# Kernel optimization log

Hardware: AMD Instinct MI355X
Metric: run time of the kernel (lower is better)

## Reference

```python
import jax, jax.numpy as jnp
import numpy as np

MIDC = 256
HEADS = 16
HEADC = MIDC // HEADS
EPS = 1e-5


def _layernorm(x, w, b):
    # Faithful to the custom torch LayerNorm: unbiased std (ddof=1) and
    # division by (std + eps), NOT sqrt(var + eps).
    mean = jnp.mean(x, axis=-1, keepdims=True)
    std = jnp.std(x, axis=-1, keepdims=True, ddof=1)
    return w * (x - mean) / (std + EPS) + b


def setup_inputs() -> dict:
    key = jax.random.key(0)
    ks = jax.random.split(key, 3)
    B, HW = 8, 16384
    x = jax.random.normal(ks[0], (B, HW, MIDC), dtype=jnp.float32)
    W_qkv = jax.random.normal(ks[1], (3 * MIDC, MIDC), dtype=jnp.float32) * 0.02
    b_qkv = jnp.zeros((3 * MIDC,), dtype=jnp.float32)
    kln_w = jnp.ones((HEADS, 1, HEADC), dtype=jnp.float32)
    kln_b = jnp.zeros((HEADS, 1, HEADC), dtype=jnp.float32)
    vln_w = jnp.ones((HEADS, 1, HEADC), dtype=jnp.float32)
    vln_b = jnp.zeros((HEADS, 1, HEADC), dtype=jnp.float32)
    W_proj = jax.random.normal(ks[2], (MIDC, MIDC), dtype=jnp.float32) * 0.02
    b_proj = jnp.zeros((MIDC,), dtype=jnp.float32)
    return {"x": x, "W_qkv": W_qkv, "b_qkv": b_qkv,
            "kln_w": kln_w, "kln_b": kln_b, "vln_w": vln_w, "vln_b": vln_b,
            "W_proj": W_proj, "b_proj": b_proj}


def reference(x, W_qkv, b_qkv, kln_w, kln_b, vln_w, vln_b, W_proj, b_proj):
    B, HW, C = x.shape
    bias = x
    # QKV projection -> [B, heads, HW, 3*headc]
    qkv = (jnp.einsum('bnc,oc->bno', x, W_qkv) + b_qkv)
    qkv = qkv.reshape(B, HW, HEADS, 3 * HEADC).transpose(0, 2, 1, 3)
    q, k, v = jnp.split(qkv, 3, axis=-1)  # each [B, heads, HW, headc]
    k = _layernorm(k, kln_w, kln_b)
    v = _layernorm(v, vln_w, vln_b)
    # linear attention: kv = k^T v / HW, then q @ kv
    kv = jnp.einsum('bhnd,bhne->bhde', k, v) / HW  # [B, heads, headc, headc]
    out = jnp.einsum('bhnd,bhde->bhne', q, kv)     # [B, heads, HW, headc]
    out = out.transpose(0, 2, 1, 3).reshape(B, HW, C)
    ret = out + bias
    proj = jnp.einsum('bnc,oc->bno', ret, W_proj) + b_proj
    return jax.nn.gelu(proj, approximate=False) + bias
```

## Files before the change

### kernel.cpp

```cpp
#include <hip/hip_runtime.h>
#include <hip/hip_bf16.h>
#include <math.h>


#define EPSF 1e-5f

typedef __bf16 bf16x8 __attribute__((ext_vector_type(8)));
typedef __bf16 bf16x4 __attribute__((ext_vector_type(4)));
typedef float  f32x4  __attribute__((ext_vector_type(4)));

__global__ void k0_prep(const float* __restrict__ Wqkv, const float* __restrict__ Wproj,
                        __bf16* __restrict__ Wkv, __bf16* __restrict__ Wp,
                        float* __restrict__ kv) {
  int idx = blockIdx.x * 256 + threadIdx.x;
  if (idx < 32768) kv[idx] = 0.f;
  {
    int r = idx >> 8, c = idx & 255;
    int half = r >> 8;
    int rr = r & 255;
    int h = rr >> 4, d = rr & 15;
    Wkv[idx] = (__bf16)Wqkv[(h*48 + 16 + half*16 + d)*256 + c];
  }
  if (idx < 65536) Wp[idx] = (__bf16)Wproj[idx];
}

__launch_bounds__(512, 4)
__global__ void k1a(const float* __restrict__ x, const __bf16* __restrict__ Wkv,
                    const float* __restrict__ bqkv,
                    const float* __restrict__ klnw, const float* __restrict__ klnb,
                    const float* __restrict__ vlnw, const float* __restrict__ vlnb,
                    float* __restrict__ kvout) {
  __shared__ __align__(16) char smem[70656];
  __bf16 (*xs)[264] = reinterpret_cast<__bf16(*)[264]>(smem);
  const int tid = threadIdx.x;
  const int w = tid >> 6, l = tid & 63, lr = l & 15, g = l >> 4;
  __bf16 (*tTk)[72] = reinterpret_cast<__bf16(*)[72]>(smem + 33792 + w*4608);
  __bf16 (*tTv)[64] = reinterpret_cast<__bf16(*)[64]>(smem + w*4096);

  const long row0 = (long)blockIdx.x * 64;
  const int b = (int)(row0 >> 14);

  #pragma unroll
  for (int i = 0; i < 8; ++i) {
    int idx = tid + i*512;
    int r = idx >> 6, c4 = (idx & 63) << 2;
    f32x4 v = *reinterpret_cast<const f32x4*>(x + (row0 + r)*256 + c4);
    bf16x4 pk; pk[0]=(__bf16)v[0]; pk[1]=(__bf16)v[1]; pk[2]=(__bf16)v[2]; pk[3]=(__bf16)v[3];
    *reinterpret_cast<bf16x4*>(&xs[r][c4]) = pk;
  }

  bf16x8 wk[2][8];
  #pragma unroll
  for (int cb=0;cb<2;cb++) {
    const __bf16* wp = Wkv + (size_t)(w*32 + cb*16 + lr)*256 + g*8;
    #pragma unroll
    for (int kc=0;kc<8;kc++) wk[cb][kc] = *reinterpret_cast<const bf16x8*>(wp + kc*32);
  }
  __syncthreads();

  f32x4 acc[2][4];
  for (int cb=0;cb<2;cb++) for (int rb=0;rb<4;rb++)
    for (int j=0;j<4;j++) acc[cb][rb][j]=0.f;
  #pragma unroll
  for (int kc = 0; kc < 8; ++kc) {
    const int kb = kc*32 + g*8;
    bf16x8 bf_[4];
    #pragma unroll
    for (int rb=0;rb<4;rb++)
      bf_[rb] = *reinterpret_cast<const bf16x8*>(&xs[rb*16+lr][kb]);
    #pragma unroll
    for (int cb=0;cb<2;cb++)
      #pragma unroll
      for (int rb=0;rb<4;rb++)
        acc[cb][rb] = __builtin_amdgcn_mfma_f32_16x16x32_bf16(wk[cb][kc], bf_[rb], acc[cb][rb], 0,0,0);
  }

  bf16x8 wv[2][8];
  #pragma unroll
  for (int cb=0;cb<2;cb++) {
    const __bf16* wp = Wkv + (size_t)(256 + w*32 + cb*16 + lr)*256 + g*8;
    #pragma unroll
    for (int kc=0;kc<8;kc++) wv[cb][kc] = *reinterpret_cast<const bf16x8*>(wp + kc*32);
  }

  #pragma unroll
  for (int cb=0;cb<2;cb++) {
    const int h = 2*w + cb;
    const f32x4 bb  = *reinterpret_cast<const f32x4*>(bqkv + h*48 + 16 + 4*g);
    const f32x4 lwv = *reinterpret_cast<const f32x4*>(klnw + h*16 + 4*g);
    const f32x4 lbv = *reinterpret_cast<const f32x4*>(klnb + h*16 + 4*g);
    #pragma unroll
    for (int rb=0;rb<4;rb++) {
      float v0 = acc[cb][rb][0] + bb[0];
      float v1 = acc[cb][rb][1] + bb[1];
      float v2 = acc[cb][rb][2] + bb[2];
      float v3 = acc[cb][rb][3] + bb[3];
      float sum = v0+v1+v2+v3;
      sum += __shfl_xor(sum, 16); sum += __shfl_xor(sum, 32);
      const float mu = sum * 0.0625f;
      const float d0=v0-mu, d1=v1-mu, d2=v2-mu, d3=v3-mu;
      float q = d0*d0 + d1*d1 + d2*d2 + d3*d3;
      q += __shfl_xor(q, 16); q += __shfl_xor(q, 32);
      const float sc = __frsqrt_rn(q * (1.f/15.f));
      const int rr = rb*16 + lr;
      tTk[cb*16 + 4*g+0][rr] = (__bf16)(lwv[0]*d0*sc + lbv[0]);
      tTk[cb*16 + 4*g+1][rr] = (__bf16)(lwv[1]*d1*sc + lbv[1]);
      tTk[cb*16 + 4*g+2][rr] = (__bf16)(lwv[2]*d2*sc + lbv[2]);
      tTk[cb*16 + 4*g+3][rr] = (__bf16)(lwv[3]*d3*sc + lbv[3]);
    }
  }

  for (int cb=0;cb<2;cb++) for (int rb=0;rb<4;rb++)
    for (int j=0;j<4;j++) acc[cb][rb][j]=0.f;
  #pragma unroll
  for (int kc = 0; kc < 8; ++kc) {
    const int kb = kc*32 + g*8;
    bf16x8 bf_[4];
    #pragma unroll
    for (int rb=0;rb<4;rb++)
      bf_[rb] = *reinterpret_cast<const bf16x8*>(&xs[rb*16+lr][kb]);
    #pragma unroll
    for (int cb=0;cb<2;cb++)
      #pragma unroll
      for (int rb=0;rb<4;rb++)
        acc[cb][rb] = __builtin_amdgcn_mfma_f32_16x16x32_bf16(wv[cb][kc], bf_[rb], acc[cb][rb], 0,0,0);
  }

  bf16x4 vpk[2][4];
  #pragma unroll
  for (int cb=0;cb<2;cb++) {
    const int h = 2*w + cb;
    const f32x4 bb  = *reinterpret_cast<const f32x4*>(bqkv + h*48 + 32 + 4*g);
    const f32x4 lwv = *reinterpret_cast<const f32x4*>(vlnw + h*16 + 4*g);
    const f32x4 lbv = *reinterpret_cast<const f32x4*>(vlnb + h*16 + 4*g);
    #pragma unroll
    for (int rb=0;rb<4;rb++) {
      float v0 = acc[cb][rb][0] + bb[0];
      float v1 = acc[cb][rb][1] + bb[1];
      float v2 = acc[cb][rb][2] + bb[2];
      float v3 = acc[cb][rb][3] + bb[3];
      float sum = v0+v1+v2+v3;
      sum += __shfl_xor(sum, 16); sum += __shfl_xor(sum, 32);
      const float mu = sum * 0.0625f;
      const float d0=v0-mu, d1=v1-mu, d2=v2-mu, d3=v3-mu;
      float q = d0*d0 + d1*d1 + d2*d2 + d3*d3;
      q += __shfl_xor(q, 16); q += __shfl_xor(q, 32);
      const float sc = __frsqrt_rn(q * (1.f/15.f));
      vpk[cb][rb][0] = (__bf16)(lwv[0]*d0*sc + lbv[0]);
      vpk[cb][rb][1] = (__bf16)(lwv[1]*d1*sc + lbv[1]);
      vpk[cb][rb][2] = (__bf16)(lwv[2]*d2*sc + lbv[2]);
      vpk[cb][rb][3] = (__bf16)(lwv[3]*d3*sc + lbv[3]);
    }
  }

  __syncthreads();

  #pragma unroll
  for (int cb=0;cb<2;cb++) {
    #pragma unroll
    for (int rb=0;rb<4;rb++) {
      const int rr = rb*16 + lr;
      tTv[cb*16 + 4*g+0][rr ^ (((4*g+0)&7)<<3)] = vpk[cb][rb][0];
      tTv[cb*16 + 4*g+1][rr ^ (((4*g+1)&7)<<3)] = vpk[cb][rb][1];
      tTv[cb*16 + 4*g+2][rr ^ (((4*g+2)&7)<<3)] = vpk[cb][rb][2];
      tTv[cb*16 + 4*g+3][rr ^ (((4*g+3)&7)<<3)] = vpk[cb][rb][3];
    }
  }

  #pragma unroll
  for (int hh=0; hh<2; ++hh) {
    f32x4 c; c[0]=0.f; c[1]=0.f; c[2]=0.f; c[3]=0.f;
    #pragma unroll
    for (int ch=0; ch<2; ++ch) {
      const int s = ch*32 + g*8;
      bf16x8 a  = *reinterpret_cast<const bf16x8*>(&tTk[hh*16 + lr][s]);
      bf16x8 bv = *reinterpret_cast<const bf16x8*>(&tTv[hh*16 + lr][s ^ ((lr&7)<<3)]);
      c = __builtin_amdgcn_mfma_f32_16x16x32_bf16(a, bv, c, 0,0,0);
    }
    float* dst = kvout + ((size_t)(b*16 + 2*w + hh) << 8);
    #pragma unroll
    for (int j=0;j<4;j++)
      atomicAdd(dst + (4*g+j)*16 + lr, c[j]);
  }
}

__global__ void k2_weff(const float* __restrict__ Wqkv, const float* __restrict__ bqkv,
                        const float* __restrict__ kvin,
                        __bf16* __restrict__ Wqe, float* __restrict__ beff) {
  const int b = blockIdx.x >> 4, h = blockIdx.x & 15;
  const int c = threadIdx.x;
  __shared__ float kvs[16][16];
  kvs[c >> 4][c & 15] = kvin[(b*16 + h)*256 + c] * (1.f/16384.f);
  __syncthreads();
  #pragma unroll 4
  for (int e=0;e<16;e++) {
    float acc = 0.f;
    #pragma unroll
    for (int d=0; d<16; d++)
      acc += kvs[d][e] * Wqkv[(h*48 + d)*256 + c];
    Wqe[((size_t)b*256 + h*16 + e)*256 + c] = (__bf16)acc;
  }
  if (c < 16) {
    float acc = 0.f;
    #pragma unroll
    for (int d=0; d<16; d++) acc += kvs[d][c] * bqkv[h*48 + d];
    beff[b*256 + h*16 + c] = acc;
  }
}

__launch_bounds__(512, 4)
__global__ void k3_fused(const float* __restrict__ x, const __bf16* __restrict__ Wqe,
                         const float* __restrict__ beff, const __bf16* __restrict__ Wp,
                         const float* __restrict__ bproj, float* __restrict__ out) {
  __shared__ __align__(16) __bf16 xs[64][264];
  __shared__ __align__(16) char rsraw[33792];
  __bf16 (*rs)[264] = reinterpret_cast<__bf16(*)[264]>(rsraw);
  float  (*fst)[260] = reinterpret_cast<float(*)[260]>(rsraw);
  const int tid = threadIdx.x;
  const long browg = (long)blockIdx.x * 64;
  const int b = (int)(browg >> 14);
  const int w = tid>>6, l = tid&63, lr = l&15, g = l>>4;

  #pragma unroll
  for (int i = 0; i < 8; ++i) {
    int idx = tid + i*512;
    int r = idx >> 6, c4 = (idx & 63) << 2;
    f32x4 v = *reinterpret_cast<const f32x4*>(x + (browg + r)*256 + c4);
    bf16x4 pk; pk[0]=(__bf16)v[0]; pk[1]=(__bf16)v[1]; pk[2]=(__bf16)v[2]; pk[3]=(__bf16)v[3];
    *reinterpret_cast<bf16x4*>(&xs[r][c4]) = pk;
  }

  const __bf16* Bq = Wqe + (size_t)b*65536;
  bf16x8 wq[2][8];
  #pragma unroll
  for (int cb=0;cb<2;cb++) {
    const __bf16* wp = Bq + (size_t)(w*32 + cb*16 + lr)*256 + g*8;
    #pragma unroll
    for (int kc=0;kc<8;kc++) wq[cb][kc] = *reinterpret_cast<const bf16x8*>(wp + kc*32);
  }
  __syncthreads();

  f32x4 acc[2][4];
  for (int cb=0;cb<2;cb++) for (int rb=0;rb<4;rb++)
    for (int j=0;j<4;j++) acc[cb][rb][j]=0.f;
  #pragma unroll
  for (int kc=0;kc<8;kc++) {
    const int kb = kc*32 + g*8;
    bf16x8 bf_[4];
    #pragma unroll
    for (int rb=0;rb<4;rb++)
      bf_[rb] = *reinterpret_cast<const bf16x8*>(&xs[rb*16+lr][kb]);
    #pragma unroll
    for (int cb=0;cb<2;cb++)
      #pragma unroll
      for (int rb=0;rb<4;rb++)
        acc[cb][rb] = __builtin_amdgcn_mfma_f32_16x16x32_bf16(wq[cb][kc], bf_[rb], acc[cb][rb], 0,0,0);
  }

  bf16x8 wpj[2][8];
  #pragma unroll
  for (int cb=0;cb<2;cb++) {
    const __bf16* wp = Wp + (size_t)(w*32 + cb*16 + lr)*256 + g*8;
    #pragma unroll
    for (int kc=0;kc<8;kc++) wpj[cb][kc] = *reinterpret_cast<const bf16x8*>(wp + kc*32);
  }

  #pragma unroll
  for (int cb=0;cb<2;cb++) {
    const int c0 = w*32 + cb*16 + 4*g;
    const f32x4 be = *reinterpret_cast<const f32x4*>(beff + b*256 + c0);
    #pragma unroll
    for (int rb=0;rb<4;rb++) {
      const int r = rb*16 + lr;
      bf16x4 xv = *reinterpret_cast<const bf16x4*>(&xs[r][c0]);
      bf16x4 pk;
      #pragma unroll
      for (int j=0;j<4;j++)
        pk[j] = (__bf16)(acc[cb][rb][j] + be[j] + (float)xv[j]);
      *reinterpret_cast<bf16x4*>(&rs[r][c0]) = pk;
    }
  }
  __syncthreads();

  f32x4 acc2[2][4];
  for (int cb=0;cb<2;cb++) for (int rb=0;rb<4;rb++)
    for (int j=0;j<4;j++) acc2[cb][rb][j]=0.f;
  #pragma unroll
  for (int kc=0;kc<8;kc++) {
    const int kb = kc*32 + g*8;
    bf16x8 bf_[4];
    #pragma unroll
    for (int rb=0;rb<4;rb++)
      bf_[rb] = *reinterpret_cast<const bf16x8*>(&rs[rb*16+lr][kb]);
    #pragma unroll
    for (int cb=0;cb<2;cb++)
      #pragma unroll
      for (int rb=0;rb<4;rb++)
        acc2[cb][rb] = __builtin_amdgcn_mfma_f32_16x16x32_bf16(wpj[cb][kc], bf_[rb], acc2[cb][rb], 0,0,0);
  }
  __syncthreads();

  #pragma unroll
  for (int half=0; half<2; ++half) {
    #pragma unroll
    for (int cb=0;cb<2;cb++) {
      const int c0 = w*32 + cb*16 + 4*g;
      const f32x4 bp4 = *reinterpret_cast<const f32x4*>(bproj + c0);
      #pragma unroll
      for (int rbh=0;rbh<2;rbh++) {
        const int rb = half*2 + rbh;
        const int r = rb*16 + lr;
        bf16x4 xv = *reinterpret_cast<const bf16x4*>(&xs[r][c0]);
        f32x4 o;
        #pragma unroll
        for (int j=0;j<4;j++) {
          float z = acc2[cb][rb][j] + bp4[j];
          o[j] = 0.5f*z*(1.f + erff(z*0.70710678118f)) + (float)xv[j];
        }
        *reinterpret_cast<f32x4*>(&fst[r - half*32][c0]) = o;
      }
    }
    __syncthreads();
    #pragma unroll
    for (int i=0;i<4;i++) {
      int idx = tid + i*512;
      int r32 = idx >> 6, c4 = (idx & 63) << 2;
      f32x4 v = *reinterpret_cast<const f32x4*>(&fst[r32][c4]);
      *reinterpret_cast<f32x4*>(out + (browg + half*32 + r32)*256 + c4) = v;
    }
    if (half == 0) __syncthreads();
  }
}

extern "C" void kernel_launch(void* const* d_in, const int* in_sizes, int n_in,
                              void* d_out, int out_size, void* d_ws, size_t ws_size,
                              hipStream_t stream) {
  const float* x    = (const float*)d_in[0];
  const float* Wqkv = (const float*)d_in[1];
  const float* bqkv = (const float*)d_in[2];
  const float* klnw = (const float*)d_in[3];
  const float* klnb = (const float*)d_in[4];
  const float* vlnw = (const float*)d_in[5];
  const float* vlnb = (const float*)d_in[6];
  const float* Wproj= (const float*)d_in[7];
  const float* bproj= (const float*)d_in[8];
  float* out = (float*)d_out;

  char* ws = (char*)d_ws;
  __bf16* Wkv = (__bf16*)(ws);
  __bf16* Wp  = (__bf16*)(ws + 262144);
  float*  kv  = (float*) (ws + 393216);
  __bf16* Wqe = (__bf16*)(ws + 524288);
  float*  beff= (float*) (ws + 1572864);

  k0_prep <<<512, 256, 0, stream>>>(Wqkv, Wproj, Wkv, Wp, kv);
  k1a     <<<2048, 512, 0, stream>>>(x, Wkv, bqkv, klnw, klnb, vlnw, vlnb, kv);
  k2_weff <<<128, 256, 0, stream>>>(Wqkv, bqkv, kv, Wqe, beff);
  k3_fused<<<2048, 512, 0, stream>>>(x, Wqe, beff, Wp, bproj, out);
}
```

Baseline: 192.5 us.

## Replace kv atomics with per-block partials reduced in k2, stream weight fragments

Each k1a block now writes its 16 per-head 16x16 kv partials to a scratch buffer carved out of the output tensor. k2_weff sums the 256 partials per batch/head, replacing the global atomicAdd accumulation and the zero-init in k0_prep. The K/V weight fragments are also loaded per k-step inside the MFMA loop rather than preloaded into 16 registers per cb, which cuts register pressure at the cost of more global/L2 loads in the inner loop. This relies on k3 fully overwriting the output afterwards, and k2 now reads about 8 MB of partials.

```diff
diff --git a/kernel.cpp b/kernel.cpp
--- a/kernel.cpp
+++ b/kernel.cpp
@@ -10,10 +10,8 @@
 typedef float  f32x4  __attribute__((ext_vector_type(4)));
 
 __global__ void k0_prep(const float* __restrict__ Wqkv, const float* __restrict__ Wproj,
-                        __bf16* __restrict__ Wkv, __bf16* __restrict__ Wp,
-                        float* __restrict__ kv) {
+                        __bf16* __restrict__ Wkv, __bf16* __restrict__ Wp) {
   int idx = blockIdx.x * 256 + threadIdx.x;
-  if (idx < 32768) kv[idx] = 0.f;
   {
     int r = idx >> 8, c = idx & 255;
     int half = r >> 8;
@@ -29,7 +27,7 @@
                     const float* __restrict__ bqkv,
                     const float* __restrict__ klnw, const float* __restrict__ klnb,
                     const float* __restrict__ vlnw, const float* __restrict__ vlnb,
-                    float* __restrict__ kvout) {
+                    float* __restrict__ part) {
   __shared__ __align__(16) char smem[70656];
   __bf16 (*xs)[264] = reinterpret_cast<__bf16(*)[264]>(smem);
   const int tid = threadIdx.x;
@@ -38,7 +36,6 @@
   __bf16 (*tTv)[64] = reinterpret_cast<__bf16(*)[64]>(smem + w*4096);
 
   const long row0 = (long)blockIdx.x * 64;
-  const int b = (int)(row0 >> 14);
 
   #pragma unroll
   for (int i = 0; i < 8; ++i) {
@@ -48,14 +45,6 @@
     bf16x4 pk; pk[0]=(__bf16)v[0]; pk[1]=(__bf16)v[1]; pk[2]=(__bf16)v[2]; pk[3]=(__bf16)v[3];
     *reinterpret_cast<bf16x4*>(&xs[r][c4]) = pk;
   }
-
-  bf16x8 wk[2][8];
-  #pragma unroll
-  for (int cb=0;cb<2;cb++) {
-    const __bf16* wp = Wkv + (size_t)(w*32 + cb*16 + lr)*256 + g*8;
-    #pragma unroll
-    for (int kc=0;kc<8;kc++) wk[cb][kc] = *reinterpret_cast<const bf16x8*>(wp + kc*32);
-  }
   __syncthreads();
 
   f32x4 acc[2][4];
@@ -64,7 +53,10 @@
   #pragma unroll
   for (int kc = 0; kc < 8; ++kc) {
     const int kb = kc*32 + g*8;
-    bf16x8 bf_[4];
+    bf16x8 wfr[2], bf_[4];
+    #pragma unroll
+    for (int cb=0;cb<2;cb++)
+      wfr[cb] = *reinterpret_cast<const bf16x8*>(Wkv + (size_t)(w*32 + cb*16 + lr)*256 + kb);
     #pragma unroll
     for (int rb=0;rb<4;rb++)
       bf_[rb] = *reinterpret_cast<const bf16x8*>(&xs[rb*16+lr][kb]);
@@ -72,15 +64,7 @@
     for (int cb=0;cb<2;cb++)
       #pragma unroll
       for (int rb=0;rb<4;rb++)
-        acc[cb][rb] = __builtin_amdgcn_mfma_f32_16x16x32_bf16(wk[cb][kc], bf_[rb], acc[cb][rb], 0,0,0);
-  }
-
-  bf16x8 wv[2][8];
-  #pragma unroll
-  for (int cb=0;cb<2;cb++) {
-    const __bf16* wp = Wkv + (size_t)(256 + w*32 + cb*16 + lr)*256 + g*8;
-    #pragma unroll
-    for (int kc=0;kc<8;kc++) wv[cb][kc] = *reinterpret_cast<const bf16x8*>(wp + kc*32);
+        acc[cb][rb] = __builtin_amdgcn_mfma_f32_16x16x32_bf16(wfr[cb], bf_[rb], acc[cb][rb], 0,0,0);
   }
 
   #pragma unroll
@@ -115,7 +99,10 @@
   #pragma unroll
   for (int kc = 0; kc < 8; ++kc) {
     const int kb = kc*32 + g*8;
-    bf16x8 bf_[4];
+    bf16x8 wfr[2], bf_[4];
+    #pragma unroll
+    for (int cb=0;cb<2;cb++)
+      wfr[cb] = *reinterpret_cast<const bf16x8*>(Wkv + (size_t)(256 + w*32 + cb*16 + lr)*256 + kb);
     #pragma unroll
     for (int rb=0;rb<4;rb++)
       bf_[rb] = *reinterpret_cast<const bf16x8*>(&xs[rb*16+lr][kb]);
@@ -123,7 +110,7 @@
     for (int cb=0;cb<2;cb++)
       #pragma unroll
       for (int rb=0;rb<4;rb++)
-        acc[cb][rb] = __builtin_amdgcn_mfma_f32_16x16x32_bf16(wv[cb][kc], bf_[rb], acc[cb][rb], 0,0,0);
+        acc[cb][rb] = __builtin_amdgcn_mfma_f32_16x16x32_bf16(wfr[cb], bf_[rb], acc[cb][rb], 0,0,0);
   }
 
   bf16x4 vpk[2][4];
@@ -177,20 +164,29 @@
       bf16x8 bv = *reinterpret_cast<const bf16x8*>(&tTv[hh*16 + lr][s ^ ((lr&7)<<3)]);
       c = __builtin_amdgcn_mfma_f32_16x16x32_bf16(a, bv, c, 0,0,0);
     }
-    float* dst = kvout + ((size_t)(b*16 + 2*w + hh) << 8);
+    float* dst = part + ((size_t)blockIdx.x*16 + 2*w + hh)*256;
     #pragma unroll
     for (int j=0;j<4;j++)
-      atomicAdd(dst + (4*g+j)*16 + lr, c[j]);
+      dst[(4*g+j)*16 + lr] = c[j];
   }
 }
 
 __global__ void k2_weff(const float* __restrict__ Wqkv, const float* __restrict__ bqkv,
-                        const float* __restrict__ kvin,
+                        const float* __restrict__ part,
                         __bf16* __restrict__ Wqe, float* __restrict__ beff) {
   const int b = blockIdx.x >> 4, h = blockIdx.x & 15;
   const int c = threadIdx.x;
   __shared__ float kvs[16][16];
-  kvs[c >> 4][c & 15] = kvin[(b*16 + h)*256 + c] * (1.f/16384.f);
+  const float* base = part + ((size_t)(b*256)*16 + h)*256 + c;
+  float a0=0.f, a1=0.f, a2=0.f, a3=0.f;
+  #pragma unroll 8
+  for (int i=0;i<256;i+=4) {
+    a0 += base[(size_t)(i+0)*4096];
+    a1 += base[(size_t)(i+1)*4096];
+    a2 += base[(size_t)(i+2)*4096];
+    a3 += base[(size_t)(i+3)*4096];
+  }
+  kvs[c >> 4][c & 15] = ((a0+a1)+(a2+a3)) * (1.f/16384.f);
   __syncthreads();
   #pragma unroll 4
   for (int e=0;e<16;e++) {
@@ -349,12 +345,13 @@
   char* ws = (char*)d_ws;
   __bf16* Wkv = (__bf16*)(ws);
   __bf16* Wp  = (__bf16*)(ws + 262144);
-  float*  kv  = (float*) (ws + 393216);
-  __bf16* Wqe = (__bf16*)(ws + 524288);
-  float*  beff= (float*) (ws + 1572864);
-
-  k0_prep <<<512, 256, 0, stream>>>(Wqkv, Wproj, Wkv, Wp, kv);
-  k1a     <<<2048, 512, 0, stream>>>(x, Wkv, bqkv, klnw, klnb, vlnw, vlnb, kv);
-  k2_weff <<<128, 256, 0, stream>>>(Wqkv, bqkv, kv, Wqe, beff);
+  __bf16* Wqe = (__bf16*)(ws + 393216);
+  float*  beff= (float*) (ws + 1441792);
+
+  float* part = (float*)d_out;
+
+  k0_prep <<<512, 256, 0, stream>>>(Wqkv, Wproj, Wkv, Wp);
+  k1a     <<<2048, 512, 0, stream>>>(x, Wkv, bqkv, klnw, klnb, vlnw, vlnb, part);
+  k2_weff <<<128, 256, 0, stream>>>(Wqkv, bqkv, part, Wqe, beff);
   k3_fused<<<2048, 512, 0, stream>>>(x, Wqe, beff, Wp, bproj, out);
 }
```

After: 213.0 us. +10.6%, slower.
